# Performance work log

Measured on AMD Instinct MI355X. Metric: run time of the kernel, lower is better.

The kernel has to match this reference:

```python
import jax, jax.numpy as jnp
import numpy as np

D, N = 512, 65536


def setup_inputs() -> dict:
    key = jax.random.key(0)
    k1, k2 = jax.random.split(key)
    feats = jax.random.normal(k1, (D, N), dtype=jnp.float32)
    warped_feats = jax.random.normal(k2, (D, N), dtype=jnp.float32)
    return {"feats": feats, "warped_feats": warped_feats}


def reference(feats, warped_feats):
    # diag(feats.T @ warped_feats)[n] == sum_d feats[d,n] * warped_feats[d,n]
    # Same math as the torch module, without materializing the NxN matrix.
    diag = jnp.einsum('dn,dn->n', feats, warped_feats)  # [N]
    cosine = 1.0 - diag
    return cosine.mean()
```

## Files before the change

### kernel.cpp

```cpp
#include <hip/hip_runtime.h>

#define THREADS 256
#define VPT 4

__global__ __launch_bounds__(THREADS) void dot_partial_kernel(
        const float4* __restrict__ a,
        const float4* __restrict__ b,
        float* __restrict__ partial) {
    const int base = blockIdx.x * (THREADS * VPT) + threadIdx.x;

    float4 xa[VPT], xb[VPT];
    #pragma unroll
    for (int j = 0; j < VPT; ++j) xa[j] = a[base + j * THREADS];
    #pragma unroll
    for (int j = 0; j < VPT; ++j) xb[j] = b[base + j * THREADS];

    float acc[VPT];
    #pragma unroll
    for (int j = 0; j < VPT; ++j) {
        acc[j] = xa[j].x * xb[j].x;
        acc[j] = fmaf(xa[j].y, xb[j].y, acc[j]);
        acc[j] = fmaf(xa[j].z, xb[j].z, acc[j]);
        acc[j] = fmaf(xa[j].w, xb[j].w, acc[j]);
    }
    float s = (acc[0] + acc[1]) + (acc[2] + acc[3]);

    #pragma unroll
    for (int off = 32; off > 0; off >>= 1)
        s += __shfl_down(s, off, 64);

    __shared__ float smem[THREADS / 64];
    int lane = threadIdx.x & 63;
    int wave = threadIdx.x >> 6;
    if (lane == 0) smem[wave] = s;
    __syncthreads();

    if (threadIdx.x == 0) {
        float t = 0.f;
        #pragma unroll
        for (int w = 0; w < THREADS / 64; ++w) t += smem[w];
        partial[blockIdx.x] = t;
    }
}

__global__ __launch_bounds__(THREADS) void final_reduce_kernel(
        const float* __restrict__ partial,
        float* __restrict__ out,
        int np, float inv_n) {
    float s = 0.f;
    for (int i = threadIdx.x; i < np; i += THREADS) s += partial[i];

    #pragma unroll
    for (int off = 32; off > 0; off >>= 1)
        s += __shfl_down(s, off, 64);

    __shared__ float smem[THREADS / 64];
    int lane = threadIdx.x & 63;
    int wave = threadIdx.x >> 6;
    if (lane == 0) smem[wave] = s;
    __syncthreads();

    if (threadIdx.x == 0) {
        float t = 0.f;
        #pragma unroll
        for (int w = 0; w < THREADS / 64; ++w) t += smem[w];
        out[0] = 1.0f - t * inv_n;
    }
}

extern "C" void kernel_launch(void* const* d_in, const int* in_sizes, int n_in,
                              void* d_out, int out_size, void* d_ws, size_t ws_size,
                              hipStream_t stream) {
    const float* feats  = (const float*)d_in[0];
    const float* warped = (const float*)d_in[1];
    float* out = (float*)d_out;
    float* ws  = (float*)d_ws;

    const long long total = (long long)in_sizes[0];
    const int n4 = (int)(total / 4);
    const int blocks = n4 / (THREADS * VPT);
    const float inv_n = 1.0f / 65536.0f;

    dot_partial_kernel<<<blocks, THREADS, 0, stream>>>(
        (const float4*)feats, (const float4*)warped, ws);
    final_reduce_kernel<<<1, THREADS, 0, stream>>>(ws, out, blocks, inv_n);
}
```

Baseline: 276.8 us.

## Use persistent grid-stride loop with nontemporal vector loads for dot reduction

Replaces one-shot blocks with a fixed grid of 1024 blocks of 512 threads, each looping 16 times with four independent accumulators and nontemporal 128-bit loads. This is meant to keep more memory requests in flight per thread and reduce the number of partial sums the final single-block reduce must read. Sizes are now hardcoded to the fixed problem shape instead of derived from input sizes.

```diff
diff --git a/kernel.cpp b/kernel.cpp
--- a/kernel.cpp
+++ b/kernel.cpp
@@ -1,37 +1,51 @@
 #include <hip/hip_runtime.h>
 
-#define THREADS 256
-#define VPT 4
+#define THREADS 512
+#define BLOCKS  1024
+#define ITERS   16
+#define UNROLL  4
+
+typedef float f32x4 __attribute__((ext_vector_type(4)));
 
 __global__ __launch_bounds__(THREADS) void dot_partial_kernel(
-        const float4* __restrict__ a,
-        const float4* __restrict__ b,
+        const f32x4* __restrict__ a,
+        const f32x4* __restrict__ b,
         float* __restrict__ partial) {
-    const int base = blockIdx.x * (THREADS * VPT) + threadIdx.x;
+    const int tid    = blockIdx.x * THREADS + threadIdx.x;
+    const int stride = THREADS * BLOCKS;
 
-    float4 xa[VPT], xb[VPT];
+    f32x4 acc0 = (f32x4)0.f, acc1 = (f32x4)0.f, acc2 = (f32x4)0.f, acc3 = (f32x4)0.f;
+
     #pragma unroll
-    for (int j = 0; j < VPT; ++j) xa[j] = a[base + j * THREADS];
-    #pragma unroll
-    for (int j = 0; j < VPT; ++j) xb[j] = b[base + j * THREADS];
+    for (int i = 0; i < ITERS; i += UNROLL) {
+        long long i0 = (long long)(i + 0) * stride + tid;
+        long long i1 = (long long)(i + 1) * stride + tid;
+        long long i2 = (long long)(i + 2) * stride + tid;
+        long long i3 = (long long)(i + 3) * stride + tid;
+        f32x4 a0 = __builtin_nontemporal_load(a + i0);
+        f32x4 b0 = __builtin_nontemporal_load(b + i0);
+        f32x4 a1 = __builtin_nontemporal_load(a + i1);
+        f32x4 b1 = __builtin_nontemporal_load(b + i1);
+        f32x4 a2 = __builtin_nontemporal_load(a + i2);
+        f32x4 b2 = __builtin_nontemporal_load(b + i2);
+        f32x4 a3 = __builtin_nontemporal_load(a + i3);
+        f32x4 b3 = __builtin_nontemporal_load(b + i3);
+        acc0 += a0 * b0;
+        acc1 += a1 * b1;
+        acc2 += a2 * b2;
+        acc3 += a3 * b3;
+    }
 
-    float acc[VPT];
-    #pragma unroll
-    for (int j = 0; j < VPT; ++j) {
-        acc[j] = xa[j].x * xb[j].x;
-        acc[j] = fmaf(xa[j].y, xb[j].y, acc[j]);
-        acc[j] = fmaf(xa[j].z, xb[j].z, acc[j]);
-        acc[j] = fmaf(xa[j].w, xb[j].w, acc[j]);
-    }
-    float s = (acc[0] + acc[1]) + (acc[2] + acc[3]);
+    f32x4 accv = (acc0 + acc1) + (acc2 + acc3);
+    float s = (accv.x + accv.y) + (accv.z + accv.w);
 
     #pragma unroll
     for (int off = 32; off > 0; off >>= 1)
         s += __shfl_down(s, off, 64);
 
     __shared__ float smem[THREADS / 64];
-    int lane = threadIdx.x & 63;
-    int wave = threadIdx.x >> 6;
+    const int lane = threadIdx.x & 63;
+    const int wave = threadIdx.x >> 6;
     if (lane == 0) smem[wave] = s;
     __syncthreads();
 
@@ -43,27 +57,27 @@
     }
 }
 
-__global__ __launch_bounds__(THREADS) void final_reduce_kernel(
+__global__ __launch_bounds__(256) void final_reduce_kernel(
         const float* __restrict__ partial,
         float* __restrict__ out,
         int np, float inv_n) {
     float s = 0.f;
-    for (int i = threadIdx.x; i < np; i += THREADS) s += partial[i];
+    for (int i = threadIdx.x; i < np; i += 256) s += partial[i];
 
     #pragma unroll
     for (int off = 32; off > 0; off >>= 1)
         s += __shfl_down(s, off, 64);
 
-    __shared__ float smem[THREADS / 64];
-    int lane = threadIdx.x & 63;
-    int wave = threadIdx.x >> 6;
+    __shared__ float smem[4];
+    const int lane = threadIdx.x & 63;
+    const int wave = threadIdx.x >> 6;
     if (lane == 0) smem[wave] = s;
     __syncthreads();
 
     if (threadIdx.x == 0) {
         float t = 0.f;
         #pragma unroll
-        for (int w = 0; w < THREADS / 64; ++w) t += smem[w];
+        for (int w = 0; w < 4; ++w) t += smem[w];
         out[0] = 1.0f - t * inv_n;
     }
 }
@@ -76,12 +90,9 @@
     float* out = (float*)d_out;
     float* ws  = (float*)d_ws;
 
-    const long long total = (long long)in_sizes[0];
-    const int n4 = (int)(total / 4);
-    const int blocks = n4 / (THREADS * VPT);
     const float inv_n = 1.0f / 65536.0f;
 
-    dot_partial_kernel<<<blocks, THREADS, 0, stream>>>(
-        (const float4*)feats, (const float4*)warped, ws);
-    final_reduce_kernel<<<1, THREADS, 0, stream>>>(ws, out, blocks, inv_n);
+    dot_partial_kernel<<<BLOCKS, THREADS, 0, stream>>>(
+        (const f32x4*)feats, (const f32x4*)warped, ws);
+    final_reduce_kernel<<<1, 256, 0, stream>>>(ws, out, BLOCKS, inv_n);
 }
```

After: 248.6 us. -10.2%, faster.
